# Kernel optimization log

Measured on AMD Instinct MI355X. Metric: run time of the kernel, lower is better.

Reference implementation:

```python
import jax, jax.numpy as jnp
import numpy as np

NUM_HEADS = 16


def setup_inputs() -> dict:
    rng = jax.random.key(0)
    ks = jax.random.split(rng, 11)
    T, B, E = 1024, 4, 1024
    s = E ** -0.5  # weight init scale
    return {
        "query": jax.random.normal(ks[0], (T, B, E), jnp.float32),
        "key": jax.random.normal(ks[1], (T, B, E), jnp.float32),
        "value": jax.random.normal(ks[2], (T, B, E), jnp.float32),
        "q_proj_weight": jax.random.normal(ks[3], (E, E), jnp.float32) * s,
        "k_proj_weight1": jax.random.normal(ks[4], (E, E), jnp.float32) * s,
        "k_proj_weight2": jax.random.normal(ks[5], (E, E), jnp.float32) * s,
        "v_proj_weight": jax.random.normal(ks[6], (E, E), jnp.float32) * s,
        "in_proj_bias": jax.random.normal(ks[7], (4 * E,), jnp.float32) * 0.02,
        "out_proj_weight": jax.random.normal(ks[8], (E, E), jnp.float32) * s,
        "out_proj_bias": jax.random.normal(ks[9], (E,), jnp.float32) * 0.02,
        "pi": jax.random.uniform(ks[10], (2, NUM_HEADS), jnp.float32, 0.3, 0.7),
    }


def reference(query, key, value, q_proj_weight, k_proj_weight1, k_proj_weight2,
              v_proj_weight, in_proj_bias, out_proj_weight, out_proj_bias, pi):
    T, Bz, E = query.shape
    H = NUM_HEADS
    hd = E // H
    scaling = hd ** -0.5

    b_q, b_k1, b_k2, b_v = jnp.split(in_proj_bias, 4)
    q = query @ q_proj_weight.T + b_q
    k1 = key @ k_proj_weight1.T + b_k1
    k2 = key @ k_proj_weight2.T + b_k2
    v = value @ v_proj_weight.T + b_v

    def heads(x):  # (S, B, E) -> (B*H, S, hd)
        S = x.shape[0]
        return x.reshape(S, Bz * H, hd).transpose(1, 0, 2)

    q, k1, k2, v = heads(q), heads(k1), heads(k2), heads(v)

    def sqdist(a, b):  # (B*H, Nt, hd), (B*H, Ns, hd) -> (B*H, Nt, Ns)
        a2 = jnp.sum(a * a, axis=-1)
        b2 = jnp.sum(b * b, axis=-1)
        ab = jnp.einsum('btd,bsd->bts', a, b)
        return a2[:, :, None] + b2[:, None, :] - 2.0 * ab

    e1 = jnp.exp(-scaling / 2.0 * sqdist(q, k1))
    e2 = jnp.exp(-3.0 * scaling / 2.0 * sqdist(q, k2))

    pi1 = jnp.clip(jnp.abs(pi[0]), 1e-6, 2.0)  # (H,)
    pi2 = jnp.clip(jnp.abs(pi[1]), 1e-6, 2.0)

    Nt, Ns = e1.shape[1], e1.shape[2]
    attn = (e1.reshape(Bz, H, Nt, Ns) * pi1[None, :, None, None]
            + e2.reshape(Bz, H, Nt, Ns) * pi2[None, :, None, None])
    attn = attn.reshape(Bz * H, Nt, Ns)
    attn = attn / (jnp.sum(attn, axis=-1, keepdims=True) + 1e-6)

    out = jnp.einsum('bts,bsd->btd', attn, v)        # (B*H, Nt, hd)
    out = out.transpose(1, 0, 2).reshape(T, Bz, E)   # (T, B, E)
    return out @ out_proj_weight.T + out_proj_bias
```

## Files before the change

### kernel.cpp

```cpp
#include <hip/hip_runtime.h>
#include <hip/hip_bf16.h>

#define T_DIM 1024
#define B_DIM 4
#define E_DIM 1024
#define H_DIM 16
#define HD    64
#define M_DIM (T_DIM * B_DIM)

typedef __hip_bfloat16 bf16;
typedef __bf16 bf16x8 __attribute__((ext_vector_type(8)));
typedef __bf16 bf16x4 __attribute__((ext_vector_type(4)));
typedef float  f32x4  __attribute__((ext_vector_type(4)));

#define P4S ((size_t)M_DIM * E_DIM)
#define P1S ((size_t)E_DIM * E_DIM)

__global__ __launch_bounds__(256) void cvt_all(
    const float* __restrict__ q, const float* __restrict__ k,
    const float* __restrict__ v, const float* __restrict__ w0,
    const float* __restrict__ w1, const float* __restrict__ w2,
    const float* __restrict__ w3, const float* __restrict__ w4,
    __bf16* __restrict__ dst)
{
  size_t i = ((size_t)blockIdx.x * 256 + threadIdx.x) * 8;
  const float* src;
  size_t off;
  if (i < P4S)            { src = q; off = i; }
  else if (i < 2 * P4S)   { src = k; off = i - P4S; }
  else if (i < 3 * P4S)   { src = v; off = i - 2 * P4S; }
  else {
    size_t j = i - 3 * P4S;
    int wsel = (int)(j >> 20);
    off = j & (P1S - 1);
    const float* ws[5] = {w0, w1, w2, w3, w4};
    src = ws[wsel];
  }
  float4 a = *(const float4*)(src + off);
  float4 b = *(const float4*)(src + off + 4);
  bf16x8 o;
  o[0] = (__bf16)a.x; o[1] = (__bf16)a.y; o[2] = (__bf16)a.z; o[3] = (__bf16)a.w;
  o[4] = (__bf16)b.x; o[5] = (__bf16)b.y; o[6] = (__bf16)b.z; o[7] = (__bf16)b.w;
  *(bf16x8*)(dst + i) = o;
}

__device__ __forceinline__ void load_lds16(const __bf16* g, __bf16* l) {
  __builtin_amdgcn_global_load_lds(
      (__attribute__((address_space(1))) void*)(void*)g,
      (__attribute__((address_space(3))) void*)l, 16, 0, 0);
}

template <typename TO>
__device__ __forceinline__ void gemm_body(
    const __bf16* __restrict__ X, const __bf16* __restrict__ W,
    const float* __restrict__ bias, TO* __restrict__ C,
    int bm, int bn, int Ndim, int Kdim, __bf16* As, __bf16* Bs)
{
  const int tid  = threadIdx.x;
  const int lane = tid & 63;
  const int wave = tid >> 6;
  const int wy = (wave >> 1) * 64;
  const int wx = (wave & 1) * 64;
  const int mrow = lane & 15, quad = lane >> 4;

  const int srow = tid >> 2;
  const int ke   = (tid & 3) * 8;
  const __bf16* gA0 = X + (size_t)(bm + srow)      * Kdim + ke;
  const __bf16* gA1 = X + (size_t)(bm + srow + 64) * Kdim + ke;
  const __bf16* gB0 = W + (size_t)(bn + srow)      * Kdim + ke;
  const __bf16* gB1 = W + (size_t)(bn + srow + 64) * Kdim + ke;
  __bf16* lA0 = As + tid * 8;
  __bf16* lA1 = As + (tid + 256) * 8;
  __bf16* lB0 = Bs + tid * 8;
  __bf16* lB1 = Bs + (tid + 256) * 8;

  f32x4 acc[4][4];
#pragma unroll
  for (int i = 0; i < 4; ++i)
#pragma unroll
    for (int j = 0; j < 4; ++j) acc[i][j] = (f32x4)0.0f;

  for (int k0 = 0; k0 < Kdim; k0 += 32) {
    __syncthreads();
    load_lds16(gA0 + k0, lA0);
    load_lds16(gA1 + k0, lA1);
    load_lds16(gB0 + k0, lB0);
    load_lds16(gB1 + k0, lB1);
    __syncthreads();
    bf16x8 af[4], bf[4];
#pragma unroll
    for (int i = 0; i < 4; ++i)
      af[i] = *(const bf16x8*)(As + (wy + i * 16 + mrow) * 32 + quad * 8);
#pragma unroll
    for (int j = 0; j < 4; ++j)
      bf[j] = *(const bf16x8*)(Bs + (wx + j * 16 + mrow) * 32 + quad * 8);
#pragma unroll
    for (int i = 0; i < 4; ++i)
#pragma unroll
      for (int j = 0; j < 4; ++j)
        acc[i][j] = __builtin_amdgcn_mfma_f32_16x16x32_bf16(af[i], bf[j], acc[i][j], 0, 0, 0);
  }

#pragma unroll
  for (int j = 0; j < 4; ++j) {
    int col = bn + wx + j * 16 + mrow;
    float bc = bias[col];
#pragma unroll
    for (int i = 0; i < 4; ++i) {
      int rbase = bm + wy + i * 16 + quad * 4;
#pragma unroll
      for (int r = 0; r < 4; ++r)
        C[(size_t)(rbase + r) * Ndim + col] = (TO)(acc[i][j][r] + bc);
    }
  }
}

__global__ __launch_bounds__(256) void proj_gemm4(
    const __bf16* __restrict__ xbase, const __bf16* __restrict__ wbase,
    const float* __restrict__ bin, __bf16* __restrict__ cbase)
{
  __shared__ __bf16 As[128 * 32];
  __shared__ __bf16 Bs[128 * 32];
  const int z = blockIdx.z;
  const __bf16* X = xbase + ((z == 0) ? 0 : (z == 3) ? 2 * P4S : P4S);
  const __bf16* W = wbase + (size_t)z * P1S;
  const float* bias = bin + z * E_DIM;
  __bf16* C = cbase + (size_t)z * P4S;
  gemm_body<__bf16>(X, W, bias, C, blockIdx.x * 128, blockIdx.y * 128,
                    E_DIM, E_DIM, As, Bs);
}

__global__ __launch_bounds__(256) void out_gemm(
    const __bf16* __restrict__ X, const __bf16* __restrict__ W,
    const float* __restrict__ bias, float* __restrict__ C)
{
  __shared__ __bf16 As[128 * 32];
  __shared__ __bf16 Bs[128 * 32];
  gemm_body<float>(X, W, bias, C, blockIdx.x * 128, blockIdx.y * 128,
                   E_DIM, E_DIM, As, Bs);
}

__global__ __launch_bounds__(256) void head_norms(
    const __bf16* __restrict__ Qp, const __bf16* __restrict__ K1p,
    const __bf16* __restrict__ K2p, float* __restrict__ qn,
    float* __restrict__ kn1, float* __restrict__ kn2)
{
  int id = blockIdx.x * 256 + threadIdx.x;
  int which = id >> 16;
  int r = id & 65535;
  int bh = r >> 10, t = r & 1023;
  int b = bh >> 4, h = bh & 15;
  const __bf16* src = (which == 0) ? Qp : ((which == 1) ? K1p : K2p);
  float* dst = (which == 0) ? qn : ((which == 1) ? kn1 : kn2);
  const __bf16* p = src + (size_t)(t * 4 + b) * 1024 + h * 64;
  float s = 0.f;
#pragma unroll
  for (int c = 0; c < 8; ++c) {
    bf16x8 v = *(const bf16x8*)(p + c * 8);
#pragma unroll
    for (int j = 0; j < 8; ++j) { float x = (float)v[j]; s += x * x; }
  }
  dst[bh * 1024 + t] = s;
}

__global__ __launch_bounds__(256) void v_transpose(
    const __bf16* __restrict__ Vp, __bf16* __restrict__ Vt_g)
{
  const int bh = blockIdx.x, kt = blockIdx.y;
  const int b = bh >> 4, h = bh & 15;
  const int tid = threadIdx.x;
  __shared__ __bf16 tile[64][88];
  {
    int s = tid >> 2, d0 = (tid & 3) * 16;
    const __bf16* src = Vp + (size_t)((kt * 64 + s) * 4 + b) * 1024 + h * 64 + d0;
    *(bf16x8*)(&tile[s][d0])     = *(const bf16x8*)(src);
    *(bf16x8*)(&tile[s][d0 + 8]) = *(const bf16x8*)(src + 8);
  }
  __syncthreads();
#pragma unroll
  for (int c = 0; c < 2; ++c) {
    int idx = tid * 2 + c;
    int d = idx >> 3, u0 = (idx & 7) * 8;
    bf16x8 o;
#pragma unroll
    for (int i = 0; i < 8; ++i) {
      int u = u0 + i;
      int s = (u & 3) * 16 + (u >> 2);
      o[i] = tile[s][d];
    }
    *(bf16x8*)(Vt_g + ((size_t)bh * 64 + d) * 1024 + kt * 64 + u0) = o;
  }
}

__global__ __launch_bounds__(256, 4) void mgk_attn_mfma(
    const __bf16* __restrict__ Qp, const __bf16* __restrict__ K1p,
    const __bf16* __restrict__ K2p, const __bf16* __restrict__ Vt_g,
    const float* __restrict__ qn_g, const float* __restrict__ kn1_g,
    const float* __restrict__ kn2_g, const float* __restrict__ pi,
    __bf16* __restrict__ AO)
{
  __shared__ __bf16 lds[16384];
  __bf16* K1s = lds;
  __bf16* K2s = lds + 4096;
  __bf16* Vt  = lds + 8192;
  __bf16* Pl  = lds + 12288;

  const int bh = blockIdx.x, qt = blockIdx.y;
  const int b = bh >> 4, h = bh & 15;
  const int tid = threadIdx.x, lane = tid & 63, w = tid >> 6;
  const int mrow = lane & 15, quad = lane >> 4;

  const float cl1 = 0.0625f * 1.4426950408889634f;
  const float cl2 = 0.1875f * 1.4426950408889634f;
  const float L1 = 2.0f * cl1, L2 = 2.0f * cl2;
  const float p1 = fminf(fmaxf(fabsf(pi[h]), 1e-6f), 2.0f);
  const float p2 = fminf(fmaxf(fabsf(pi[H_DIM + h]), 1e-6f), 2.0f);
  const int hoff = h * 64;

  bf16x8 af[2];
  {
    const __bf16* qp = Qp + (size_t)((qt * 64 + w * 16 + mrow) * 4 + b) * 1024
                       + hoff + quad * 8;
    af[0] = *(const bf16x8*)(qp);
    af[1] = *(const bf16x8*)(qp + 32);
  }
  f32x4 qnv = *(const f32x4*)(qn_g + bh * 1024 + qt * 64 + w * 16 + quad * 4);
  f32x4 ncq1, ncq2;
#pragma unroll
  for (int r = 0; r < 4; ++r) { ncq1[r] = -cl1 * qnv[r]; ncq2[r] = -cl2 * qnv[r]; }

  f32x4 oacc[4];
#pragma unroll
  for (int j = 0; j < 4; ++j) oacc[j] = (f32x4)0.0f;
  f32x4 rsl = (f32x4)0.0f;

  for (int kt = 0; kt < 16; ++kt) {
    __syncthreads();
#pragma unroll
    for (int wi = 0; wi < 2; ++wi) {
      int window = w * 2 + wi;
      int kr = window * 8 + (lane >> 3), c = lane & 7;
      size_t srow = (size_t)((kt * 64 + kr) * 4 + b) * 1024 + hoff;
      int off = (c ^ (kr & 7)) << 3;
      load_lds16(K1p + srow + off, K1s + window * 512 + lane * 8);
      load_lds16(K2p + srow + off, K2s + window * 512 + lane * 8);
      load_lds16(Vt_g + ((size_t)bh * 64 + kr) * 1024 + kt * 64 + off,
                 Vt + window * 512 + lane * 8);
    }
    float kn1j[4], kn2j[4];
#pragma unroll
    for (int j = 0; j < 4; ++j) {
      kn1j[j] = kn1_g[bh * 1024 + kt * 64 + j * 16 + mrow];
      kn2j[j] = kn2_g[bh * 1024 + kt * 64 + j * 16 + mrow];
    }
    __syncthreads();

    f32x4 acc1[4], acc2[4];
#pragma unroll
    for (int j = 0; j < 4; ++j) { acc1[j] = (f32x4)0.0f; acc2[j] = (f32x4)0.0f; }
#pragma unroll
    for (int kk = 0; kk < 2; ++kk)
#pragma unroll
      for (int j = 0; j < 4; ++j) {
        bf16x8 b1f = *(const bf16x8*)(K1s + (j * 16 + mrow) * 64
                                      + (((kk * 4 + quad) ^ (mrow & 7)) << 3));
        bf16x8 b2f = *(const bf16x8*)(K2s + (j * 16 + mrow) * 64
                                      + (((kk * 4 + quad) ^ (mrow & 7)) << 3));
        acc1[j] = __builtin_amdgcn_mfma_f32_16x16x32_bf16(af[kk], b1f, acc1[j], 0, 0, 0);
        acc2[j] = __builtin_amdgcn_mfma_f32_16x16x32_bf16(af[kk], b2f, acc2[j], 0, 0, 0);
      }

    f32x4 pv[4];
#pragma unroll
    for (int j = 0; j < 4; ++j) {
      f32x4 p;
#pragma unroll
      for (int r = 0; r < 4; ++r) {
        float e1 = __builtin_amdgcn_exp2f(fmaf(L1, acc1[j][r], fmaf(-cl1, kn1j[j], ncq1[r])));
        float e2 = __builtin_amdgcn_exp2f(fmaf(L2, acc2[j][r], fmaf(-cl2, kn2j[j], ncq2[r])));
        p[r] = fmaf(p2, e2, p1 * e1);
      }
      pv[j] = p;
      rsl += p;
    }
#pragma unroll
    for (int r = 0; r < 4; ++r) {
      int q = quad * 4 + r;
      bf16x4 pk;
      pk[0] = (__bf16)pv[0][r]; pk[1] = (__bf16)pv[1][r];
      pk[2] = (__bf16)pv[2][r]; pk[3] = (__bf16)pv[3][r];
      int lc = mrow >> 1;
      *(bf16x4*)(Pl + w * 1024 + q * 64 + ((lc ^ (q & 7)) << 3) + (mrow & 1) * 4) = pk;
    }

    bf16x8 pf[2];
#pragma unroll
    for (int kk = 0; kk < 2; ++kk)
      pf[kk] = *(const bf16x8*)(Pl + w * 1024 + mrow * 64
                                + (((kk * 4 + quad) ^ (mrow & 7)) << 3));
#pragma unroll
    for (int kk = 0; kk < 2; ++kk)
#pragma unroll
      for (int j = 0; j < 4; ++j) {
        bf16x8 vf = *(const bf16x8*)(Vt + (j * 16 + mrow) * 64
                                     + (((kk * 4 + quad) ^ (mrow & 7)) << 3));
        oacc[j] = __builtin_amdgcn_mfma_f32_16x16x32_bf16(pf[kk], vf, oacc[j], 0, 0, 0);
      }
  }

#pragma unroll
  for (int d = 1; d < 16; d <<= 1) {
    f32x4 o;
#pragma unroll
    for (int r = 0; r < 4; ++r) o[r] = __shfl_xor(rsl[r], d, 64);
    rsl += o;
  }

  f32x4 inv;
#pragma unroll
  for (int r = 0; r < 4; ++r) inv[r] = 1.0f / (rsl[r] + 1e-6f);
#pragma unroll
  for (int j = 0; j < 4; ++j) {
    int col = hoff + j * 16 + mrow;
#pragma unroll
    for (int r = 0; r < 4; ++r) {
      int t = qt * 64 + w * 16 + quad * 4 + r;
      AO[(size_t)(t * 4 + b) * 1024 + col] = (__bf16)(oacc[j][r] * inv[r]);
    }
  }
}

extern "C" void kernel_launch(void* const* d_in, const int* in_sizes, int n_in,
                              void* d_out, int out_size, void* d_ws, size_t ws_size,
                              hipStream_t stream) {
  const float* query = (const float*)d_in[0];
  const float* key   = (const float*)d_in[1];
  const float* value = (const float*)d_in[2];
  const float* Wq    = (const float*)d_in[3];
  const float* Wk1   = (const float*)d_in[4];
  const float* Wk2   = (const float*)d_in[5];
  const float* Wv    = (const float*)d_in[6];
  const float* bin   = (const float*)d_in[7];
  const float* Wo    = (const float*)d_in[8];
  const float* bo    = (const float*)d_in[9];
  const float* pi    = (const float*)d_in[10];
  float* out = (float*)d_out;

  __bf16* qc  = (__bf16*)d_ws;
  __bf16* wq  = qc  + 3 * P4S;
  __bf16* wo  = wq  + 4 * P1S;
  __bf16* Qp  = wq  + 5 * P1S;
  __bf16* K1p = Qp  + P4S;
  __bf16* K2p = K1p + P4S;
  __bf16* Vp  = K2p + P4S;
  __bf16* AO  = Vp  + P4S;
  float*  qn_g  = (float*)(AO + P4S);
  float*  kn1_g = qn_g  + 64 * 1024;
  float*  kn2_g = kn1_g + 64 * 1024;
  __bf16* Vt_g  = qc;

  cvt_all<<<8704, 256, 0, stream>>>(query, key, value, Wq, Wk1, Wk2, Wv, Wo, qc);

  proj_gemm4<<<dim3(M_DIM / 128, E_DIM / 128, 4), 256, 0, stream>>>(qc, wq, bin, Qp);

  head_norms<<<768, 256, 0, stream>>>(Qp, K1p, K2p, qn_g, kn1_g, kn2_g);
  v_transpose<<<dim3(64, 16), 256, 0, stream>>>(Vp, Vt_g);

  mgk_attn_mfma<<<dim3(64, 16), 256, 0, stream>>>(
      Qp, K1p, K2p, Vt_g, qn_g, kn1_g, kn2_g, pi, AO);

  out_gemm<<<dim3(M_DIM / 128, E_DIM / 128), 256, 0, stream>>>(AO, wo, bo, out);
}
```

Measured before the change: 270.4 us.

## Rewrite projection GEMM with 256x256 tiles, double-buffered swizzled LDS and staged prefetch

Replaces the 128x128, 256-thread projection GEMM with a 512-thread kernel that computes 256x256 tiles with a K-step of 64. Operands are staged into double-buffered, XOR-swizzled LDS through direct global-to-LDS loads, and the prefetch is split into quarter-stages placed between MFMA phases. The kernel also raises wave priority around the MFMA bursts. The aim is more data reuse per tile, fewer LDS bank conflicts, and global loads that overlap compute. The cost is 128 KB of LDS per block, heavy register use, a smaller grid (256 blocks), and fragile hand-coded waitcnt and barrier scheduling.

```diff
diff --git a/kernel.cpp b/kernel.cpp
--- a/kernel.cpp
+++ b/kernel.cpp
@@ -50,6 +50,168 @@
       (__attribute__((address_space(3))) void*)l, 16, 0, 0);
 }
 
+__device__ __forceinline__ void stage_half(
+    int H, const __bf16* __restrict__ X, const __bf16* __restrict__ W,
+    int bm, int bn, __bf16* As, __bf16* Bs, int tid)
+{
+  if (H >= 64) return;
+  const int T  = H >> 2;
+  const int h  = H & 3;
+  const int rh = (h & 1) * 128;
+  const __bf16* src = (h < 2) ? X : W;
+  const int rbase   = (h < 2) ? bm : bn;
+  __bf16* lb = ((h < 2) ? As : Bs) + (T & 1) * 16384;
+#pragma unroll
+  for (int li = 0; li < 2; ++li) {
+    int r  = rh + li * 64 + (tid >> 3);
+    int gc = (tid & 7) ^ (r & 7);
+    load_lds16(src + (size_t)(rbase + r) * E_DIM + T * 64 + gc * 8,
+               lb + (rh + li * 64) * 64 + tid * 8);
+  }
+}
+
+#define RD(base, row, c) \
+  (*(const bf16x8*)((base) + (row) * 64 + ((((c) ^ ((row) & 7))) << 3)))
+
+__global__ __launch_bounds__(512, 2) void proj_gemm4(
+    const __bf16* __restrict__ xbase, const __bf16* __restrict__ wbase,
+    const float* __restrict__ bin, __bf16* __restrict__ cbase)
+{
+  __shared__ __bf16 lds[65536];
+  __bf16* As = lds;
+  __bf16* Bs = lds + 32768;
+
+  const int z = blockIdx.z;
+  const __bf16* X = xbase + ((z == 0) ? 0 : (z == 3) ? 2 * P4S : P4S);
+  const __bf16* W = wbase + (size_t)z * P1S;
+  const float* bias = bin + z * E_DIM;
+  __bf16* C = cbase + (size_t)z * P4S;
+
+  const int bm = blockIdx.x * 256;
+  const int bn = blockIdx.y * 256;
+
+  const int tid  = threadIdx.x;
+  const int lane = tid & 63;
+  const int w    = tid >> 6;
+  const int wm   = w >> 2;
+  const int wn   = w & 3;
+  const int mrow = lane & 15, quad = lane >> 4;
+
+  f32x4 acc[8][4];
+#pragma unroll
+  for (int m = 0; m < 8; ++m)
+#pragma unroll
+    for (int n = 0; n < 4; ++n) acc[m][n] = (f32x4)0.0f;
+
+#pragma unroll
+  for (int H = 0; H < 5; ++H) stage_half(H, X, W, bm, bn, As, Bs, tid);
+  asm volatile("s_waitcnt vmcnt(2)" ::: "memory");
+  __builtin_amdgcn_s_barrier();
+
+  bf16x8 af[4][2];
+  bf16x8 bq[4][2];
+
+#pragma unroll 2
+  for (int t = 0; t < 16; ++t) {
+    const __bf16* Ab = As + (t & 1) * 16384;
+    const __bf16* Bb = Bs + (t & 1) * 16384;
+
+#pragma unroll
+    for (int n = 0; n < 2; ++n)
+#pragma unroll
+      for (int kk = 0; kk < 2; ++kk)
+        bq[n][kk] = RD(Bb, wn * 64 + n * 16 + mrow, kk * 4 + quad);
+#pragma unroll
+    for (int m = 0; m < 4; ++m)
+#pragma unroll
+      for (int kk = 0; kk < 2; ++kk)
+        af[m][kk] = RD(Ab, wm * 128 + m * 16 + mrow, kk * 4 + quad);
+    stage_half(4 * t + 5, X, W, bm, bn, As, Bs, tid);
+    __builtin_amdgcn_s_barrier();
+    asm volatile("s_waitcnt lgkmcnt(0)" ::: "memory");
+    __builtin_amdgcn_s_setprio(1);
+#pragma unroll
+    for (int kk = 0; kk < 2; ++kk)
+#pragma unroll
+      for (int n = 0; n < 2; ++n)
+#pragma unroll
+        for (int m = 0; m < 4; ++m)
+          acc[m][n] = __builtin_amdgcn_mfma_f32_16x16x32_bf16(
+              af[m][kk], bq[n][kk], acc[m][n], 0, 0, 0);
+    __builtin_amdgcn_s_setprio(0);
+    __builtin_amdgcn_s_barrier();
+
+#pragma unroll
+    for (int n = 2; n < 4; ++n)
+#pragma unroll
+      for (int kk = 0; kk < 2; ++kk)
+        bq[n][kk] = RD(Bb, wn * 64 + n * 16 + mrow, kk * 4 + quad);
+    stage_half(4 * t + 6, X, W, bm, bn, As, Bs, tid);
+    __builtin_amdgcn_s_barrier();
+    asm volatile("s_waitcnt lgkmcnt(0)" ::: "memory");
+    __builtin_amdgcn_s_setprio(1);
+#pragma unroll
+    for (int kk = 0; kk < 2; ++kk)
+#pragma unroll
+      for (int n = 2; n < 4; ++n)
+#pragma unroll
+        for (int m = 0; m < 4; ++m)
+          acc[m][n] = __builtin_amdgcn_mfma_f32_16x16x32_bf16(
+              af[m][kk], bq[n][kk], acc[m][n], 0, 0, 0);
+    __builtin_amdgcn_s_setprio(0);
+    __builtin_amdgcn_s_barrier();
+
+#pragma unroll
+    for (int m = 0; m < 4; ++m)
+#pragma unroll
+      for (int kk = 0; kk < 2; ++kk)
+        af[m][kk] = RD(Ab, wm * 128 + 64 + m * 16 + mrow, kk * 4 + quad);
+    stage_half(4 * t + 7, X, W, bm, bn, As, Bs, tid);
+    __builtin_amdgcn_s_barrier();
+    asm volatile("s_waitcnt lgkmcnt(0)" ::: "memory");
+    __builtin_amdgcn_s_setprio(1);
+#pragma unroll
+    for (int kk = 0; kk < 2; ++kk)
+#pragma unroll
+      for (int n = 0; n < 2; ++n)
+#pragma unroll
+        for (int m = 0; m < 4; ++m)
+          acc[4 + m][n] = __builtin_amdgcn_mfma_f32_16x16x32_bf16(
+              af[m][kk], bq[n][kk], acc[4 + m][n], 0, 0, 0);
+    __builtin_amdgcn_s_setprio(0);
+    __builtin_amdgcn_s_barrier();
+
+    stage_half(4 * t + 8, X, W, bm, bn, As, Bs, tid);
+    __builtin_amdgcn_s_barrier();
+    __builtin_amdgcn_s_setprio(1);
+#pragma unroll
+    for (int kk = 0; kk < 2; ++kk)
+#pragma unroll
+      for (int n = 2; n < 4; ++n)
+#pragma unroll
+        for (int m = 0; m < 4; ++m)
+          acc[4 + m][n] = __builtin_amdgcn_mfma_f32_16x16x32_bf16(
+              af[m][kk], bq[n][kk], acc[4 + m][n], 0, 0, 0);
+    __builtin_amdgcn_s_setprio(0);
+    if (t < 14)       { asm volatile("s_waitcnt vmcnt(2)" ::: "memory"); }
+    else if (t == 14) { asm volatile("s_waitcnt vmcnt(0)" ::: "memory"); }
+    __builtin_amdgcn_s_barrier();
+  }
+
+#pragma unroll
+  for (int n = 0; n < 4; ++n) {
+    int col = bn + wn * 64 + n * 16 + mrow;
+    float bc = bias[col];
+#pragma unroll
+    for (int m = 0; m < 8; ++m) {
+      int rbase = bm + wm * 128 + m * 16 + quad * 4;
+#pragma unroll
+      for (int r = 0; r < 4; ++r)
+        C[(size_t)(rbase + r) * E_DIM + col] = (__bf16)(acc[m][n][r] + bc);
+    }
+  }
+}
+
 template <typename TO>
 __device__ __forceinline__ void gemm_body(
     const __bf16* __restrict__ X, const __bf16* __restrict__ W,
@@ -113,21 +275,6 @@
         C[(size_t)(rbase + r) * Ndim + col] = (TO)(acc[i][j][r] + bc);
     }
   }
-}
-
-__global__ __launch_bounds__(256) void proj_gemm4(
-    const __bf16* __restrict__ xbase, const __bf16* __restrict__ wbase,
-    const float* __restrict__ bin, __bf16* __restrict__ cbase)
-{
-  __shared__ __bf16 As[128 * 32];
-  __shared__ __bf16 Bs[128 * 32];
-  const int z = blockIdx.z;
-  const __bf16* X = xbase + ((z == 0) ? 0 : (z == 3) ? 2 * P4S : P4S);
-  const __bf16* W = wbase + (size_t)z * P1S;
-  const float* bias = bin + z * E_DIM;
-  __bf16* C = cbase + (size_t)z * P4S;
-  gemm_body<__bf16>(X, W, bias, C, blockIdx.x * 128, blockIdx.y * 128,
-                    E_DIM, E_DIM, As, Bs);
 }
 
 __global__ __launch_bounds__(256) void out_gemm(
@@ -361,7 +508,7 @@
 
   cvt_all<<<8704, 256, 0, stream>>>(query, key, value, Wq, Wk1, Wk2, Wv, Wo, qc);
 
-  proj_gemm4<<<dim3(M_DIM / 128, E_DIM / 128, 4), 256, 0, stream>>>(qc, wq, bin, Qp);
+  proj_gemm4<<<dim3(M_DIM / 256, E_DIM / 256, 4), 512, 0, stream>>>(qc, wq, bin, Qp);
 
   head_norms<<<768, 256, 0, stream>>>(Qp, K1p, K2p, qn_g, kn1_g, kn2_g);
   v_transpose<<<dim3(64, 16), 256, 0, stream>>>(Vp, Vt_g);
```

After: 261.3 us. -3.4%, faster.
